# Performance work log

Measured on AMD Instinct MI355X. Metric: run time of the kernel, lower is better.

## Reference

```python
import jax, jax.numpy as jnp
import numpy as np

N, E = 50000, 800000          # nodes, edges (avg degree 16)
D_IN, D_H = 128, 128          # input_size, hidden_size


def setup_inputs() -> dict:
    key = jax.random.key(0)
    ks = jax.random.split(key, 10)
    s = 0.05  # param init scale
    return {
        "x": jax.random.normal(ks[0], (N, D_IN), jnp.float32),
        "edge_index": jax.random.randint(ks[1], (2, E), 0, N, jnp.int32),
        "h_prev": jax.random.normal(ks[2], (N, D_H), jnp.float32),
        # reset gate params: xr (Linear with bias), hr (no bias)
        "W_xr": jax.random.normal(ks[3], (D_IN, D_H), jnp.float32) * s,
        "b_xr": jnp.zeros((D_H,), jnp.float32),
        "W_hr": jax.random.normal(ks[4], (D_H, D_H), jnp.float32) * s,
        # update gate params
        "W_xz": jax.random.normal(ks[5], (D_IN, D_H), jnp.float32) * s,
        "b_xz": jnp.zeros((D_H,), jnp.float32),
        "W_hz": jax.random.normal(ks[6], (D_H, D_H), jnp.float32) * s,
        # SAGEConv params: lin_l on mean-aggregated neighbors (bias), lin_r on root (no bias)
        "W_l": jax.random.normal(ks[7], (D_IN + D_H, D_H), jnp.float32) * s,
        "b_l": jnp.zeros((D_H,), jnp.float32),
        "W_r": jax.random.normal(ks[8], (D_IN + D_H, D_H), jnp.float32) * s,
    }


def reference(x, edge_index, h_prev, W_xr, b_xr, W_hr, W_xz, b_xz, W_hz, W_l, b_l, W_r):
    # GRU-style gates
    r = jax.nn.sigmoid(x @ W_xr + b_xr + h_prev @ W_hr)   # [N, D_H]
    z = jax.nn.sigmoid(x @ W_xz + b_xz + h_prev @ W_hz)   # [N, D_H]

    # candidate via single-layer GraphSAGE (SAGEConv, mean aggregation)
    xc = jnp.concatenate([x, r * h_prev], axis=-1)        # [N, D_IN+D_H]
    src, dst = edge_index[0], edge_index[1]
    agg = jax.ops.segment_sum(xc[src], dst, num_segments=N)              # [N, D_IN+D_H]
    cnt = jax.ops.segment_sum(jnp.ones((E,), xc.dtype), dst, num_segments=N)
    mean_nbr = agg / jnp.maximum(cnt, 1.0)[:, None]
    # PyG BasicGNN applies no activation after the last (only) layer, so no tanh here.
    n = mean_nbr @ W_l + b_l + xc @ W_r                   # [N, D_H]

    return (1.0 - z) * n + z * h_prev
```

## Files before the change

### kernel.cpp

```cpp
#include <hip/hip_runtime.h>
#include <hip/hip_bf16.h>

typedef __attribute__((ext_vector_type(8))) short bf16x8;
typedef __attribute__((ext_vector_type(4))) short s16x4;
typedef __attribute__((ext_vector_type(4))) float f32x4;
typedef __attribute__((ext_vector_type(4))) int i32x4;
typedef unsigned short u16;
typedef unsigned int u32;

#define D 128
#define DC 256
#define TILES 8
#define SWZ(row, dim) (((row) << 7) + ((dim) ^ (((row) & 15) << 3)))

__device__ __forceinline__ float bf2f(u16 b) {
    u32 u = ((u32)b) << 16;
    return __uint_as_float(u);
}
__device__ __forceinline__ u16 f2bf(float f) {
    u32 u = __float_as_uint(f);
    u32 r = (u + 0x7fffu + ((u >> 16) & 1u)) >> 16;
    return (u16)r;
}
__device__ __forceinline__ float sigmoidf_(float x) {
    float e = __builtin_amdgcn_exp2f(-1.4426950408889634f * x);
    return __builtin_amdgcn_rcpf(1.0f + e);
}
__device__ __forceinline__ bf16x8 cvt8(const float* __restrict__ p) {
    f32x4 lo = *(const f32x4*)p;
    f32x4 hi = *(const f32x4*)(p + 4);
    union { bf16x8 v; u16 s[8]; } u;
#pragma unroll
    for (int i = 0; i < 4; i++) {
        u.s[i]     = f2bf(lo[i]);
        u.s[i + 4] = f2bf(hi[i]);
    }
    return u.v;
}

__global__ __launch_bounds__(256) void prep_kernel(
    const float* __restrict__ Wxr, const float* __restrict__ Whr,
    const float* __restrict__ Wxz, const float* __restrict__ Whz,
    const float* __restrict__ Wl,  const float* __restrict__ Wr,
    u16* __restrict__ WxrT, u16* __restrict__ WhrT,
    u16* __restrict__ WxzT, u16* __restrict__ WhzT,
    u16* __restrict__ WlT,  u16* __restrict__ WrT,
    const int* __restrict__ ei, int* __restrict__ deg,
    int E)
{
    int bid = blockIdx.x;
    int tid = threadIdx.x;
    if (bid < 64) {
        int m = bid >> 4;
        int idx = (bid & 15) * 1024 + tid * 4;
        const float* W = (m == 0) ? Wxr : (m == 1) ? Whr : (m == 2) ? Wxz : Whz;
        u16* Wt        = (m == 0) ? WxrT : (m == 1) ? WhrT : (m == 2) ? WxzT : WhzT;
        f32x4 v = *(const f32x4*)(W + idx);
        int k = idx >> 7, n = idx & 127;
#pragma unroll
        for (int j = 0; j < 4; j++) Wt[(n + j) * D + k] = f2bf(v[j]);
    } else if (bid < 128) {
        int m = (bid - 64) >> 5;
        int idx = ((bid - 64) & 31) * 1024 + tid * 4;
        const float* W = (m == 0) ? Wl : Wr;
        u16* Wt        = (m == 0) ? WlT : WrT;
        f32x4 v = *(const f32x4*)(W + idx);
        int k = idx >> 7, n = idx & 127;
#pragma unroll
        for (int j = 0; j < 4; j++) Wt[(n + j) * DC + k] = f2bf(v[j]);
    } else {
        long long e = ((long long)(bid - 128) * 256 + tid) * 4;
        if (e + 3 < E) {
            i32x4 d4 = *(const i32x4*)(ei + (size_t)E + e);
#pragma unroll
            for (int j = 0; j < 4; j++) atomicAdd(&deg[d4[j]], 1);
        } else {
            for (int j = 0; j < 4 && e + j < E; j++)
                atomicAdd(&deg[ei[(size_t)E + e + j]], 1);
        }
    }
}

__global__ __launch_bounds__(256) void scan1_kernel(
    const int* __restrict__ deg, int* __restrict__ rstart,
    int* __restrict__ bsum, int N)
{
    __shared__ int tmp[256];
    int t = threadIdx.x;
    int g = blockIdx.x * 256 + t;
    int v = (g < N) ? deg[g] : 0;
    tmp[t] = v;
    __syncthreads();
#pragma unroll
    for (int s = 1; s < 256; s <<= 1) {
        int add = (t >= s) ? tmp[t - s] : 0;
        __syncthreads();
        tmp[t] += add;
        __syncthreads();
    }
    if (g < N) rstart[g] = tmp[t] - v;
    if (t == 255) bsum[blockIdx.x] = tmp[255];
}

__global__ __launch_bounds__(256) void scan23_kernel(
    int* __restrict__ rstart, const int* __restrict__ bsum, int N, int nbn)
{
    __shared__ int tmp[256];
    int t = threadIdx.x;
    int v = (t < nbn) ? bsum[t] : 0;
    tmp[t] = v;
    __syncthreads();
#pragma unroll
    for (int s = 1; s < 256; s <<= 1) {
        int add = (t >= s) ? tmp[t - s] : 0;
        __syncthreads();
        tmp[t] += add;
        __syncthreads();
    }
    int b = blockIdx.x;
    int excl = tmp[b] - ((b < nbn) ? bsum[b] : 0);
    int g = b * 256 + t;
    if (g < N) rstart[g] += excl;
}

__global__ __launch_bounds__(256) void fill_kernel(
    const int* __restrict__ ei, int* __restrict__ rstart,
    int* __restrict__ col, int E)
{
    long long e = ((long long)blockIdx.x * 256 + threadIdx.x) * 4;
    if (e + 3 < E) {
        i32x4 s4 = *(const i32x4*)(ei + e);
        i32x4 d4 = *(const i32x4*)(ei + (size_t)E + e);
#pragma unroll
        for (int j = 0; j < 4; j++) {
            int pos = atomicAdd(&rstart[d4[j]], 1);
            col[pos] = s4[j];
        }
    } else {
        for (long long q = e; q < E; q++) {
            int pos = atomicAdd(&rstart[ei[(size_t)E + q]], 1);
            col[pos] = ei[q];
        }
    }
}

__global__ __launch_bounds__(512, 4) void fused_kernel(
    const float* __restrict__ x, const float* __restrict__ h,
    const u16* __restrict__ WxrT, const u16* __restrict__ WhrT,
    const u16* __restrict__ WxzT, const u16* __restrict__ WhzT,
    const u16* __restrict__ WlT,  const u16* __restrict__ WrT,
    const float* __restrict__ bxr, const float* __restrict__ bxz,
    u16* __restrict__ zo, u16* __restrict__ yo, u16* __restrict__ wo, int N)
{
    __shared__ u16 xT[TILES][16 * 128];
    __shared__ u16 hT[TILES][16 * 128];
    const int wave = threadIdx.x >> 6;
    const int lane = threadIdx.x & 63;
    const int quad = lane >> 4;
    const int l15  = lane & 15;
    const int node0 = blockIdx.x * (TILES * 16);
    if (node0 >= N) return;

    {
        int tb = node0 + wave * 16;
        u16* Lx = xT[wave];
        u16* Lh = hT[wave];
#pragma unroll
        for (int it = 0; it < 4; it++) {
            int idx = it * 64 + lane;
            int row = idx >> 4, seg = idx & 15;
            int node = tb + row; if (node >= N) node = N - 1;
            *(bf16x8*)&Lx[SWZ(row, seg * 8)] = cvt8(x + (size_t)node * D + seg * 8);
            *(bf16x8*)&Lh[SWZ(row, seg * 8)] = cvt8(h + (size_t)node * D + seg * 8);
        }
    }
    __syncthreads();

    const int dim = wave * 16 + l15;
    u32 rhp0[TILES], rhp1[TILES];

    {
        const u16* wrx = WxrT + (size_t)dim * D + quad * 8;
        const u16* wrh = WhrT + (size_t)dim * D + quad * 8;
        const u16* wzx = WxzT + (size_t)dim * D + quad * 8;
        const u16* wzh = WhzT + (size_t)dim * D + quad * 8;
        bf16x8 b0[4], b1[4], b2[4], b3[4];
#pragma unroll
        for (int c = 0; c < 4; c++) {
            b0[c] = *(const bf16x8*)(wrx + c * 32);
            b1[c] = *(const bf16x8*)(wrh + c * 32);
            b2[c] = *(const bf16x8*)(wzx + c * 32);
            b3[c] = *(const bf16x8*)(wzh + c * 32);
        }
        float br = bxr[dim];
        float bz = bxz[dim];
#pragma unroll
        for (int t = 0; t < TILES; t++) {
            const u16* Lx = xT[t];
            const u16* Lh = hT[t];
            int tb = node0 + t * 16;
            bf16x8 ax[4], ah[4];
#pragma unroll
            for (int c = 0; c < 4; c++) {
                ax[c] = *(const bf16x8*)&Lx[SWZ(l15, c * 32 + quad * 8)];
                ah[c] = *(const bf16x8*)&Lh[SWZ(l15, c * 32 + quad * 8)];
            }
            f32x4 ar = {0.f,0.f,0.f,0.f};
            f32x4 az = {0.f,0.f,0.f,0.f};
#pragma unroll
            for (int c = 0; c < 4; c++) {
                ar = __builtin_amdgcn_mfma_f32_16x16x32_bf16(ax[c], b0[c], ar, 0, 0, 0);
                ar = __builtin_amdgcn_mfma_f32_16x16x32_bf16(ah[c], b1[c], ar, 0, 0, 0);
                az = __builtin_amdgcn_mfma_f32_16x16x32_bf16(ax[c], b2[c], az, 0, 0, 0);
                az = __builtin_amdgcn_mfma_f32_16x16x32_bf16(ah[c], b3[c], az, 0, 0, 0);
            }
            u32 p0 = 0, p1 = 0;
#pragma unroll
            for (int reg = 0; reg < 4; reg++) {
                int row = quad * 4 + reg;
                int node = tb + row;
                float hv = bf2f(Lh[SWZ(row, dim)]);
                float r  = sigmoidf_(ar[reg] + br);
                float zz = sigmoidf_(az[reg] + bz);
                u32 rh = f2bf(r * hv);
                if (reg == 0) p0 = rh;
                else if (reg == 1) p0 |= rh << 16;
                else if (reg == 2) p1 = rh;
                else p1 |= rh << 16;
                if (node < N) zo[(size_t)node * D + dim] = f2bf(zz);
            }
            rhp0[t] = p0;
            rhp1[t] = p1;
        }
    }
    __syncthreads();

#pragma unroll
    for (int t = 0; t < TILES; t++) {
        u16* Lh = hT[t];
        Lh[SWZ(quad * 4 + 0, dim)] = (u16)(rhp0[t]);
        Lh[SWZ(quad * 4 + 1, dim)] = (u16)(rhp0[t] >> 16);
        Lh[SWZ(quad * 4 + 2, dim)] = (u16)(rhp1[t]);
        Lh[SWZ(quad * 4 + 3, dim)] = (u16)(rhp1[t] >> 16);
    }
    __syncthreads();

    {
        const u16* pl = WlT + (size_t)dim * DC + quad * 8;
        const u16* pr = WrT + (size_t)dim * DC + quad * 8;
        bf16x8 l0[4], l1[4], r0[4], r1[4];
#pragma unroll
        for (int c = 0; c < 4; c++) {
            l0[c] = *(const bf16x8*)(pl + c * 32);
            l1[c] = *(const bf16x8*)(pl + 128 + c * 32);
            r0[c] = *(const bf16x8*)(pr + c * 32);
            r1[c] = *(const bf16x8*)(pr + 128 + c * 32);
        }
#pragma unroll
        for (int t = 0; t < TILES; t++) {
            const u16* Lx  = xT[t];
            const u16* Lrh = hT[t];
            int tb = node0 + t * 16;
            bf16x8 ax[4], arh[4];
#pragma unroll
            for (int c = 0; c < 4; c++) {
                ax[c]  = *(const bf16x8*)&Lx[SWZ(l15, c * 32 + quad * 8)];
                arh[c] = *(const bf16x8*)&Lrh[SWZ(l15, c * 32 + quad * 8)];
            }
            f32x4 ay = {0.f,0.f,0.f,0.f};
            f32x4 aw = {0.f,0.f,0.f,0.f};
#pragma unroll
            for (int c = 0; c < 4; c++) {
                ay = __builtin_amdgcn_mfma_f32_16x16x32_bf16(ax[c],  l0[c], ay, 0, 0, 0);
                ay = __builtin_amdgcn_mfma_f32_16x16x32_bf16(arh[c], l1[c], ay, 0, 0, 0);
                aw = __builtin_amdgcn_mfma_f32_16x16x32_bf16(ax[c],  r0[c], aw, 0, 0, 0);
                aw = __builtin_amdgcn_mfma_f32_16x16x32_bf16(arh[c], r1[c], aw, 0, 0, 0);
            }
#pragma unroll
            for (int reg = 0; reg < 4; reg++) {
                int row = quad * 4 + reg;
                int node = tb + row;
                if (node < N) {
                    yo[(size_t)node * D + dim] = f2bf(ay[reg]);
                    wo[(size_t)node * D + dim] = f2bf(aw[reg]);
                }
            }
        }
    }
}

__global__ __launch_bounds__(256) void pull_kernel(
    const int* __restrict__ rend, const int* __restrict__ deg,
    const int* __restrict__ col, const u16* __restrict__ y,
    const u16* __restrict__ z, const u16* __restrict__ w,
    const float* __restrict__ h, const float* __restrict__ bl,
    float* __restrict__ out, int N)
{
    const int wave = threadIdx.x >> 6;
    const int lane = threadIdx.x & 63;
    const int node = blockIdx.x * 4 + wave;
    if (node >= N) return;

    const int d    = deg[node];
    const int base = rend[node] - d;
    const int g    = lane >> 4;
    const int l15  = lane & 15;

    const int dcap = (d < 64) ? d : 64;
    int cols = 0;
    if (lane < dcap) cols = col[base + lane];

    float a[8] = {0.f,0.f,0.f,0.f,0.f,0.f,0.f,0.f};
    for (int i = 0; i < dcap; i += 8) {
        int e0 = i + g, e1 = i + 4 + g;
        int s0 = __shfl(cols, e0 & 63, 64);
        int s1 = __shfl(cols, e1 & 63, 64);
        bool v0 = e0 < dcap, v1 = e1 < dcap;
        bf16x8 A = {}, B = {};
        if (v0) A = *(const bf16x8*)(y + (size_t)s0 * D + l15 * 8);
        if (v1) B = *(const bf16x8*)(y + (size_t)s1 * D + l15 * 8);
        if (v0) {
#pragma unroll
            for (int j = 0; j < 8; j++) a[j] += bf2f((u16)A[j]);
        }
        if (v1) {
#pragma unroll
            for (int j = 0; j < 8; j++) a[j] += bf2f((u16)B[j]);
        }
    }
    for (int i = 64; i < d; i += 4) {
        int e = i + g;
        if (e < d) {
            int s = col[base + e];
            bf16x8 v = *(const bf16x8*)(y + (size_t)s * D + l15 * 8);
#pragma unroll
            for (int j = 0; j < 8; j++) a[j] += bf2f((u16)v[j]);
        }
    }
#pragma unroll
    for (int j = 0; j < 8; j++) {
        a[j] += __shfl_xor(a[j], 16, 64);
        a[j] += __shfl_xor(a[j], 32, 64);
    }
    if (lane < 16) {
        float inv = 1.0f / (float)(d > 0 ? d : 1);
        size_t o16 = (size_t)node * D + l15 * 8;
        bf16x8 zv = *(const bf16x8*)(z + o16);
        bf16x8 wv = *(const bf16x8*)(w + o16);
        f32x4 h0 = *(const f32x4*)(h + o16);
        f32x4 h1 = *(const f32x4*)(h + o16 + 4);
        f32x4 b0 = *(const f32x4*)(bl + l15 * 8);
        f32x4 b1 = *(const f32x4*)(bl + l15 * 8 + 4);
        f32x4 o0, o1;
#pragma unroll
        for (int j = 0; j < 4; j++) {
            float zz = bf2f((u16)zv[j]);
            float nv = a[j] * inv + b0[j] + bf2f((u16)wv[j]);
            o0[j] = (1.0f - zz) * nv + zz * h0[j];
        }
#pragma unroll
        for (int j = 0; j < 4; j++) {
            float zz = bf2f((u16)zv[j + 4]);
            float nv = a[j + 4] * inv + b1[j] + bf2f((u16)wv[j + 4]);
            o1[j] = (1.0f - zz) * nv + zz * h1[j];
        }
        *(f32x4*)(out + o16)     = o0;
        *(f32x4*)(out + o16 + 4) = o1;
    }
}

extern "C" void kernel_launch(void* const* d_in, const int* in_sizes, int n_in,
                              void* d_out, int out_size, void* d_ws, size_t ws_size,
                              hipStream_t stream)
{
    const float* x   = (const float*)d_in[0];
    const int*   ei  = (const int*)d_in[1];
    const float* h   = (const float*)d_in[2];
    const float* Wxr = (const float*)d_in[3];
    const float* bxr = (const float*)d_in[4];
    const float* Whr = (const float*)d_in[5];
    const float* Wxz = (const float*)d_in[6];
    const float* bxz = (const float*)d_in[7];
    const float* Whz = (const float*)d_in[8];
    const float* Wl  = (const float*)d_in[9];
    const float* bl  = (const float*)d_in[10];
    const float* Wr  = (const float*)d_in[11];
    float* out = (float*)d_out;

    const int N = in_sizes[0] / D;
    const int E = in_sizes[1] / 2;
    if (N <= 0 || E <= 0) return;

    const int nbn = (N + 255) / 256;
    if (nbn > 256) return;

    char* ws = (char*)d_ws;
    size_t off = 0;
    auto alloc = [&](size_t bytes) -> void* {
        void* p = ws + off;
        off += (bytes + 255) & ~(size_t)255;
        return p;
    };
    u16*   z     = (u16*)  alloc((size_t)N * D * 2);
    u16*   y     = (u16*)  alloc((size_t)N * D * 2);
    u16*   w     = (u16*)  alloc((size_t)N * D * 2);
    int*   deg   = (int*)  alloc((size_t)N * 4);
    int*   rstart= (int*)  alloc((size_t)N * 4);
    int*   bsum  = (int*)  alloc((size_t)256 * 4);
    int*   col   = (int*)  alloc((size_t)E * 4);
    u16*   WxrT  = (u16*)  alloc((size_t)D * D * 2);
    u16*   WhrT  = (u16*)  alloc((size_t)D * D * 2);
    u16*   WxzT  = (u16*)  alloc((size_t)D * D * 2);
    u16*   WhzT  = (u16*)  alloc((size_t)D * D * 2);
    u16*   WlT   = (u16*)  alloc((size_t)DC * D * 2);
    u16*   WrT   = (u16*)  alloc((size_t)DC * D * 2);
    (void)n_in; (void)out_size;
    if (off > ws_size) return;

    hipMemsetAsync(deg, 0, (size_t)N * 4, stream);

    const int nbh4 = (E + 1023) / 1024;
    prep_kernel<<<128 + nbh4, 256, 0, stream>>>(
        Wxr, Whr, Wxz, Whz, Wl, Wr,
        WxrT, WhrT, WxzT, WhzT, WlT, WrT,
        ei, deg, E);

    scan1_kernel<<<nbn, 256, 0, stream>>>(deg, rstart, bsum, N);
    scan23_kernel<<<nbn, 256, 0, stream>>>(rstart, bsum, N, nbn);
    fill_kernel<<<nbh4, 256, 0, stream>>>(ei, rstart, col, E);

    fused_kernel<<<(N + TILES * 16 - 1) / (TILES * 16), 512, 0, stream>>>(
        x, h, WxrT, WhrT, WxzT, WhzT, WlT, WrT, bxr, bxz, z, y, w, N);

    pull_kernel<<<(N + 3) / 4, 256, 0, stream>>>(
        rstart, deg, col, y, z, w, h, bl, out, N);
}
```

Measured before the change: 285.5 us.

## Fuse scan passes with decoupled lookback, merge fill into GEMM kernel, coalesce stores

Replaces the two-kernel block scan with a single-pass decoupled-lookback scan using tagged 64-bit state words, zeroed together with deg in one memset. It folds the CSR fill into the fused GEMM kernel as extra leading blocks, which removes a launch and lets the atomic fill overlap the matrix work. The z/y/w outputs are staged through shared memory so they go out as coalesced 16-byte row stores instead of scattered 2-byte stores, and the Wl and Wr GEMMs are split into separate passes. The pull kernel prefetches its epilogue operands and unrolls the gather to four rows per step. The changes add register pressure and rely on the lookback spin-wait, which assumes lower-indexed blocks are scheduled first.

```diff
diff --git a/kernel.cpp b/kernel.cpp
--- a/kernel.cpp
+++ b/kernel.cpp
@@ -7,6 +7,7 @@
 typedef __attribute__((ext_vector_type(4))) int i32x4;
 typedef unsigned short u16;
 typedef unsigned int u32;
+typedef unsigned long long u64;
 
 #define D 128
 #define DC 256
@@ -81,13 +82,15 @@
     }
 }
 
-__global__ __launch_bounds__(256) void scan1_kernel(
+__global__ __launch_bounds__(256) void scan_kernel(
     const int* __restrict__ deg, int* __restrict__ rstart,
-    int* __restrict__ bsum, int N)
+    u64* __restrict__ state, int N)
 {
     __shared__ int tmp[256];
-    int t = threadIdx.x;
-    int g = blockIdx.x * 256 + t;
+    __shared__ int s_excl;
+    const int c = blockIdx.x;
+    const int t = threadIdx.x;
+    int g = c * 256 + t;
     int v = (g < N) ? deg[g] : 0;
     tmp[t] = v;
     __syncthreads();
@@ -98,53 +101,38 @@
         tmp[t] += add;
         __syncthreads();
     }
-    if (g < N) rstart[g] = tmp[t] - v;
-    if (t == 255) bsum[blockIdx.x] = tmp[255];
-}
-
-__global__ __launch_bounds__(256) void scan23_kernel(
-    int* __restrict__ rstart, const int* __restrict__ bsum, int N, int nbn)
-{
-    __shared__ int tmp[256];
-    int t = threadIdx.x;
-    int v = (t < nbn) ? bsum[t] : 0;
-    tmp[t] = v;
-    __syncthreads();
-#pragma unroll
-    for (int s = 1; s < 256; s <<= 1) {
-        int add = (t >= s) ? tmp[t - s] : 0;
-        __syncthreads();
-        tmp[t] += add;
-        __syncthreads();
-    }
-    int b = blockIdx.x;
-    int excl = tmp[b] - ((b < nbn) ? bsum[b] : 0);
-    int g = b * 256 + t;
-    if (g < N) rstart[g] += excl;
-}
-
-__global__ __launch_bounds__(256) void fill_kernel(
+    int total = tmp[255];
+    if (t == 0) {
+        if (c == 0) {
+            __hip_atomic_store(&state[0], (2ull << 32) | (u32)total,
+                               __ATOMIC_RELEASE, __HIP_MEMORY_SCOPE_AGENT);
+            s_excl = 0;
+        } else {
+            __hip_atomic_store(&state[c], (1ull << 32) | (u32)total,
+                               __ATOMIC_RELEASE, __HIP_MEMORY_SCOPE_AGENT);
+            long long sum = 0;
+            int j = c - 1;
+            while (j >= 0) {
+                u64 s = __hip_atomic_load(&state[j],
+                        __ATOMIC_ACQUIRE, __HIP_MEMORY_SCOPE_AGENT);
+                u32 tag = (u32)(s >> 32);
+                if (tag == 0) continue;
+                sum += (u32)s;
+                if (tag == 2) break;
+                j--;
+            }
+            s_excl = (int)sum;
+            __hip_atomic_store(&state[c], (2ull << 32) | (u32)(sum + total),
+                               __ATOMIC_RELEASE, __HIP_MEMORY_SCOPE_AGENT);
+        }
+    }
+    __syncthreads();
+    if (g < N) rstart[g] = s_excl + tmp[t] - v;
+}
+
+__global__ __launch_bounds__(512, 4) void fillfused_kernel(
     const int* __restrict__ ei, int* __restrict__ rstart,
-    int* __restrict__ col, int E)
-{
-    long long e = ((long long)blockIdx.x * 256 + threadIdx.x) * 4;
-    if (e + 3 < E) {
-        i32x4 s4 = *(const i32x4*)(ei + e);
-        i32x4 d4 = *(const i32x4*)(ei + (size_t)E + e);
-#pragma unroll
-        for (int j = 0; j < 4; j++) {
-            int pos = atomicAdd(&rstart[d4[j]], 1);
-            col[pos] = s4[j];
-        }
-    } else {
-        for (long long q = e; q < E; q++) {
-            int pos = atomicAdd(&rstart[ei[(size_t)E + q]], 1);
-            col[pos] = ei[q];
-        }
-    }
-}
-
-__global__ __launch_bounds__(512, 4) void fused_kernel(
+    int* __restrict__ col, int E, int nbf,
     const float* __restrict__ x, const float* __restrict__ h,
     const u16* __restrict__ WxrT, const u16* __restrict__ WhrT,
     const u16* __restrict__ WxzT, const u16* __restrict__ WhzT,
@@ -152,13 +140,32 @@
     const float* __restrict__ bxr, const float* __restrict__ bxz,
     u16* __restrict__ zo, u16* __restrict__ yo, u16* __restrict__ wo, int N)
 {
+    if (blockIdx.x < nbf) {
+        long long e = ((long long)blockIdx.x * 512 + threadIdx.x) * 4;
+        if (e + 3 < E) {
+            i32x4 s4 = *(const i32x4*)(ei + e);
+            i32x4 d4 = *(const i32x4*)(ei + (size_t)E + e);
+#pragma unroll
+            for (int j = 0; j < 4; j++) {
+                int pos = atomicAdd(&rstart[d4[j]], 1);
+                col[pos] = s4[j];
+            }
+        } else {
+            for (long long q = e; q < E; q++) {
+                int pos = atomicAdd(&rstart[ei[(size_t)E + q]], 1);
+                col[pos] = ei[q];
+            }
+        }
+        return;
+    }
+
     __shared__ u16 xT[TILES][16 * 128];
     __shared__ u16 hT[TILES][16 * 128];
     const int wave = threadIdx.x >> 6;
     const int lane = threadIdx.x & 63;
     const int quad = lane >> 4;
     const int l15  = lane & 15;
-    const int node0 = blockIdx.x * (TILES * 16);
+    const int node0 = (blockIdx.x - nbf) * (TILES * 16);
     if (node0 >= N) return;
 
     {
@@ -178,6 +185,9 @@
 
     const int dim = wave * 16 + l15;
     u32 rhp0[TILES], rhp1[TILES];
+    u32 zp0[TILES],  zp1[TILES];
+    u32 yp0[TILES],  yp1[TILES];
+    u32 wp0[TILES],  wp1[TILES];
 
     {
         const u16* wrx = WxrT + (size_t)dim * D + quad * 8;
@@ -198,7 +208,6 @@
         for (int t = 0; t < TILES; t++) {
             const u16* Lx = xT[t];
             const u16* Lh = hT[t];
-            int tb = node0 + t * 16;
             bf16x8 ax[4], ah[4];
 #pragma unroll
             for (int c = 0; c < 4; c++) {
@@ -214,23 +223,22 @@
                 az = __builtin_amdgcn_mfma_f32_16x16x32_bf16(ax[c], b2[c], az, 0, 0, 0);
                 az = __builtin_amdgcn_mfma_f32_16x16x32_bf16(ah[c], b3[c], az, 0, 0, 0);
             }
-            u32 p0 = 0, p1 = 0;
+            u32 p0 = 0, p1 = 0, q0 = 0, q1 = 0;
 #pragma unroll
             for (int reg = 0; reg < 4; reg++) {
                 int row = quad * 4 + reg;
-                int node = tb + row;
                 float hv = bf2f(Lh[SWZ(row, dim)]);
                 float r  = sigmoidf_(ar[reg] + br);
                 float zz = sigmoidf_(az[reg] + bz);
                 u32 rh = f2bf(r * hv);
-                if (reg == 0) p0 = rh;
-                else if (reg == 1) p0 |= rh << 16;
-                else if (reg == 2) p1 = rh;
-                else p1 |= rh << 16;
-                if (node < N) zo[(size_t)node * D + dim] = f2bf(zz);
-            }
-            rhp0[t] = p0;
-            rhp1[t] = p1;
+                u32 zb = f2bf(zz);
+                if (reg == 0)      { p0 = rh;        q0 = zb; }
+                else if (reg == 1) { p0 |= rh << 16; q0 |= zb << 16; }
+                else if (reg == 2) { p1 = rh;        q1 = zb; }
+                else               { p1 |= rh << 16; q1 |= zb << 16; }
+            }
+            rhp0[t] = p0; rhp1[t] = p1;
+            zp0[t]  = q0; zp1[t]  = q1;
         }
     }
     __syncthreads();
@@ -247,20 +255,16 @@
 
     {
         const u16* pl = WlT + (size_t)dim * DC + quad * 8;
-        const u16* pr = WrT + (size_t)dim * DC + quad * 8;
-        bf16x8 l0[4], l1[4], r0[4], r1[4];
+        bf16x8 l0[4], l1[4];
 #pragma unroll
         for (int c = 0; c < 4; c++) {
             l0[c] = *(const bf16x8*)(pl + c * 32);
             l1[c] = *(const bf16x8*)(pl + 128 + c * 32);
-            r0[c] = *(const bf16x8*)(pr + c * 32);
-            r1[c] = *(const bf16x8*)(pr + 128 + c * 32);
         }
 #pragma unroll
         for (int t = 0; t < TILES; t++) {
             const u16* Lx  = xT[t];
             const u16* Lrh = hT[t];
-            int tb = node0 + t * 16;
             bf16x8 ax[4], arh[4];
 #pragma unroll
             for (int c = 0; c < 4; c++) {
@@ -268,23 +272,97 @@
                 arh[c] = *(const bf16x8*)&Lrh[SWZ(l15, c * 32 + quad * 8)];
             }
             f32x4 ay = {0.f,0.f,0.f,0.f};
-            f32x4 aw = {0.f,0.f,0.f,0.f};
 #pragma unroll
             for (int c = 0; c < 4; c++) {
                 ay = __builtin_amdgcn_mfma_f32_16x16x32_bf16(ax[c],  l0[c], ay, 0, 0, 0);
                 ay = __builtin_amdgcn_mfma_f32_16x16x32_bf16(arh[c], l1[c], ay, 0, 0, 0);
+            }
+            u32 p0 = f2bf(ay[0]) | ((u32)f2bf(ay[1]) << 16);
+            u32 p1 = f2bf(ay[2]) | ((u32)f2bf(ay[3]) << 16);
+            yp0[t] = p0; yp1[t] = p1;
+        }
+    }
+
+    {
+        const u16* pr = WrT + (size_t)dim * DC + quad * 8;
+        bf16x8 r0[4], r1[4];
+#pragma unroll
+        for (int c = 0; c < 4; c++) {
+            r0[c] = *(const bf16x8*)(pr + c * 32);
+            r1[c] = *(const bf16x8*)(pr + 128 + c * 32);
+        }
+#pragma unroll
+        for (int t = 0; t < TILES; t++) {
+            const u16* Lx  = xT[t];
+            const u16* Lrh = hT[t];
+            bf16x8 ax[4], arh[4];
+#pragma unroll
+            for (int c = 0; c < 4; c++) {
+                ax[c]  = *(const bf16x8*)&Lx[SWZ(l15, c * 32 + quad * 8)];
+                arh[c] = *(const bf16x8*)&Lrh[SWZ(l15, c * 32 + quad * 8)];
+            }
+            f32x4 aw = {0.f,0.f,0.f,0.f};
+#pragma unroll
+            for (int c = 0; c < 4; c++) {
                 aw = __builtin_amdgcn_mfma_f32_16x16x32_bf16(ax[c],  r0[c], aw, 0, 0, 0);
                 aw = __builtin_amdgcn_mfma_f32_16x16x32_bf16(arh[c], r1[c], aw, 0, 0, 0);
             }
-#pragma unroll
-            for (int reg = 0; reg < 4; reg++) {
-                int row = quad * 4 + reg;
-                int node = tb + row;
-                if (node < N) {
-                    yo[(size_t)node * D + dim] = f2bf(ay[reg]);
-                    wo[(size_t)node * D + dim] = f2bf(aw[reg]);
-                }
-            }
+            u32 p0 = f2bf(aw[0]) | ((u32)f2bf(aw[1]) << 16);
+            u32 p1 = f2bf(aw[2]) | ((u32)f2bf(aw[3]) << 16);
+            wp0[t] = p0; wp1[t] = p1;
+        }
+    }
+    __syncthreads();
+
+#pragma unroll
+    for (int t = 0; t < TILES; t++) {
+        u16* Zx = xT[t];
+        u16* Yh = hT[t];
+        Zx[SWZ(quad * 4 + 0, dim)] = (u16)(zp0[t]);
+        Zx[SWZ(quad * 4 + 1, dim)] = (u16)(zp0[t] >> 16);
+        Zx[SWZ(quad * 4 + 2, dim)] = (u16)(zp1[t]);
+        Zx[SWZ(quad * 4 + 3, dim)] = (u16)(zp1[t] >> 16);
+        Yh[SWZ(quad * 4 + 0, dim)] = (u16)(yp0[t]);
+        Yh[SWZ(quad * 4 + 1, dim)] = (u16)(yp0[t] >> 16);
+        Yh[SWZ(quad * 4 + 2, dim)] = (u16)(yp1[t]);
+        Yh[SWZ(quad * 4 + 3, dim)] = (u16)(yp1[t] >> 16);
+    }
+    __syncthreads();
+    {
+        int tb = node0 + wave * 16;
+        const u16* Zx = xT[wave];
+        const u16* Yh = hT[wave];
+#pragma unroll
+        for (int it = 0; it < 4; it++) {
+            int idx = it * 64 + lane;
+            int row = idx >> 4, seg = idx & 15;
+            int node = tb + row;
+            if (node < N) {
+                *(bf16x8*)(zo + (size_t)node * D + seg * 8) = *(const bf16x8*)&Zx[SWZ(row, seg * 8)];
+                *(bf16x8*)(yo + (size_t)node * D + seg * 8) = *(const bf16x8*)&Yh[SWZ(row, seg * 8)];
+            }
+        }
+    }
+    __syncthreads();
+#pragma unroll
+    for (int t = 0; t < TILES; t++) {
+        u16* Wx = xT[t];
+        Wx[SWZ(quad * 4 + 0, dim)] = (u16)(wp0[t]);
+        Wx[SWZ(quad * 4 + 1, dim)] = (u16)(wp0[t] >> 16);
+        Wx[SWZ(quad * 4 + 2, dim)] = (u16)(wp1[t]);
+        Wx[SWZ(quad * 4 + 3, dim)] = (u16)(wp1[t] >> 16);
+    }
+    __syncthreads();
+    {
+        int tb = node0 + wave * 16;
+        const u16* Wx = xT[wave];
+#pragma unroll
+        for (int it = 0; it < 4; it++) {
+            int idx = it * 64 + lane;
+            int row = idx >> 4, seg = idx & 15;
+            int node = tb + row;
+            if (node < N)
+                *(bf16x8*)(wo + (size_t)node * D + seg * 8) = *(const bf16x8*)&Wx[SWZ(row, seg * 8)];
         }
     }
 }
@@ -305,20 +383,36 @@
     const int base = rend[node] - d;
     const int g    = lane >> 4;
     const int l15  = lane & 15;
+    const size_t o16 = (size_t)node * D + l15 * 8;
+
+    bf16x8 zv = {}, wv = {};
+    f32x4 h0 = {}, h1 = {}, b0 = {}, b1 = {};
+    if (lane < 16) {
+        zv = *(const bf16x8*)(z + o16);
+        wv = *(const bf16x8*)(w + o16);
+        h0 = *(const f32x4*)(h + o16);
+        h1 = *(const f32x4*)(h + o16 + 4);
+        b0 = *(const f32x4*)(bl + l15 * 8);
+        b1 = *(const f32x4*)(bl + l15 * 8 + 4);
+    }
 
     const int dcap = (d < 64) ? d : 64;
     int cols = 0;
     if (lane < dcap) cols = col[base + lane];
 
     float a[8] = {0.f,0.f,0.f,0.f,0.f,0.f,0.f,0.f};
-    for (int i = 0; i < dcap; i += 8) {
-        int e0 = i + g, e1 = i + 4 + g;
+    for (int i = 0; i < dcap; i += 16) {
+        int e0 = i + g, e1 = i + 4 + g, e2 = i + 8 + g, e3 = i + 12 + g;
         int s0 = __shfl(cols, e0 & 63, 64);
         int s1 = __shfl(cols, e1 & 63, 64);
-        bool v0 = e0 < dcap, v1 = e1 < dcap;
-        bf16x8 A = {}, B = {};
-        if (v0) A = *(const bf16x8*)(y + (size_t)s0 * D + l15 * 8);
-        if (v1) B = *(const bf16x8*)(y + (size_t)s1 * D + l15 * 8);
+        int s2 = __shfl(cols, e2 & 63, 64);
+        int s3 = __shfl(cols, e3 & 63, 64);
+        bool v0 = e0 < dcap, v1 = e1 < dcap, v2 = e2 < dcap, v3 = e3 < dcap;
+        bf16x8 A = {}, B = {}, C = {}, Dv = {};
+        if (v0) A  = *(const bf16x8*)(y + (size_t)s0 * D + l15 * 8);
+        if (v1) B  = *(const bf16x8*)(y + (size_t)s1 * D + l15 * 8);
+        if (v2) C  = *(const bf16x8*)(y + (size_t)s2 * D + l15 * 8);
+        if (v3) Dv = *(const bf16x8*)(y + (size_t)s3 * D + l15 * 8);
         if (v0) {
 #pragma unroll
             for (int j = 0; j < 8; j++) a[j] += bf2f((u16)A[j]);
@@ -326,6 +420,14 @@
         if (v1) {
 #pragma unroll
             for (int j = 0; j < 8; j++) a[j] += bf2f((u16)B[j]);
+        }
+        if (v2) {
+#pragma unroll
+            for (int j = 0; j < 8; j++) a[j] += bf2f((u16)C[j]);
+        }
+        if (v3) {
+#pragma unroll
+            for (int j = 0; j < 8; j++) a[j] += bf2f((u16)Dv[j]);
         }
     }
     for (int i = 64; i < d; i += 4) {
@@ -344,13 +446,6 @@
     }
     if (lane < 16) {
         float inv = 1.0f / (float)(d > 0 ? d : 1);
-        size_t o16 = (size_t)node * D + l15 * 8;
-        bf16x8 zv = *(const bf16x8*)(z + o16);
-        bf16x8 wv = *(const bf16x8*)(w + o16);
-        f32x4 h0 = *(const f32x4*)(h + o16);
-        f32x4 h1 = *(const f32x4*)(h + o16 + 4);
-        f32x4 b0 = *(const f32x4*)(bl + l15 * 8);
-        f32x4 b1 = *(const f32x4*)(bl + l15 * 8 + 4);
         f32x4 o0, o1;
 #pragma unroll
         for (int j = 0; j < 4; j++) {
@@ -405,8 +500,8 @@
     u16*   y     = (u16*)  alloc((size_t)N * D * 2);
     u16*   w     = (u16*)  alloc((size_t)N * D * 2);
     int*   deg   = (int*)  alloc((size_t)N * 4);
+    u64*   state = (u64*)  alloc((size_t)256 * 8);
     int*   rstart= (int*)  alloc((size_t)N * 4);
-    int*   bsum  = (int*)  alloc((size_t)256 * 4);
     int*   col   = (int*)  alloc((size_t)E * 4);
     u16*   WxrT  = (u16*)  alloc((size_t)D * D * 2);
     u16*   WhrT  = (u16*)  alloc((size_t)D * D * 2);
@@ -417,7 +512,7 @@
     (void)n_in; (void)out_size;
     if (off > ws_size) return;
 
-    hipMemsetAsync(deg, 0, (size_t)N * 4, stream);
+    hipMemsetAsync(deg, 0, (size_t)((char*)rstart - (char*)deg), stream);
 
     const int nbh4 = (E + 1023) / 1024;
     prep_kernel<<<128 + nbh4, 256, 0, stream>>>(
@@ -425,11 +520,12 @@
         WxrT, WhrT, WxzT, WhzT, WlT, WrT,
         ei, deg, E);
 
-    scan1_kernel<<<nbn, 256, 0, stream>>>(deg, rstart, bsum, N);
-    scan23_kernel<<<nbn, 256, 0, stream>>>(rstart, bsum, N, nbn);
-    fill_kernel<<<nbh4, 256, 0, stream>>>(ei, rstart, col, E);
-
-    fused_kernel<<<(N + TILES * 16 - 1) / (TILES * 16), 512, 0, stream>>>(
+    scan_kernel<<<nbn, 256, 0, stream>>>(deg, rstart, state, N);
+
+    const int nbf = (E + 2047) / 2048;
+    const int nfu = (N + TILES * 16 - 1) / (TILES * 16);
+    fillfused_kernel<<<nbf + nfu, 512, 0, stream>>>(
+        ei, rstart, col, E, nbf,
         x, h, WxrT, WhrT, WxzT, WhzT, WlT, WrT, bxr, bxz, z, y, w, N);
 
     pull_kernel<<<(N + 3) / 4, 256, 0, stream>>>(
```

After: 330.0 us. 1.16x slower.
